# Optimization experiments

Measured on AMD Instinct MI355X. Metric: run time of the kernel, lower is better.

## Reference

```python
import jax, jax.numpy as jnp
import numpy as np

B, D, CL, QL = 32, 128, 1024, 512


def setup_inputs() -> dict:
    key = jax.random.key(0)
    kC, kQ, kW = jax.random.split(key, 3)
    C = jax.random.normal(kC, (B, D, CL), dtype=jnp.float32)
    Q = jax.random.normal(kQ, (B, D, QL), dtype=jnp.float32)
    # xavier_normal_ on (B*CL, 1, 3D): std = sqrt(2 / (fan_in + fan_out)) = sqrt(2/(1+3D))
    std = (2.0 / (1.0 + 3.0 * D)) ** 0.5
    W = jax.random.normal(kW, (B * CL, 1, 3 * D), dtype=jnp.float32) * std
    return {"C": C, "Q": Q, "W": W}


def reference(C, Q, W):
    # C: (B, D, CL), Q: (B, D, QL), W: (B*CL, 1, 3D)
    b, d, cl = C.shape
    Ct = jnp.transpose(C, (0, 2, 1))   # (B, CL, D)
    Qt = jnp.transpose(Q, (0, 2, 1))   # (B, QL, D)
    Wr = W.reshape(b, cl, 3 * d)
    wq, wc, wqc = Wr[..., :d], Wr[..., d:2 * d], Wr[..., 2 * d:]
    # Trilinear similarity: S[b,c,q] = wq[b,c].Q[b,q] + wc[b,c].C[b,c] + wqc[b,c].(C[b,c]*Q[b,q])
    S = (jnp.einsum('bcd,bqd->bcq', wq, Qt)
         + jnp.sum(wc * Ct, axis=-1, keepdims=True)
         + jnp.einsum('bcd,bqd->bcq', wqc * Ct, Qt))   # (B, CL, QL)
    S1 = jax.nn.softmax(S, axis=2)  # over queries
    S2 = jax.nn.softmax(S, axis=1)  # over context
    A = jnp.einsum('bcq,bqd->bcd', S1, Qt)             # (B, CL, D)
    # B = (S1 @ S2^T) @ C, reassociated as S1 @ (S2^T @ C) to avoid (CL,CL) intermediate
    S2tC = jnp.einsum('bkq,bkd->bqd', S2, Ct)          # (B, QL, D)
    Bm = jnp.einsum('bcq,bqd->bcd', S1, S2tC)          # (B, CL, D)
    out = jnp.concatenate([Ct, A, Ct * A, Ct * Bm], axis=2)  # (B, CL, 4D)
    # dropout is identity in eval mode
    return jnp.transpose(out, (0, 2, 1))               # (B, 4D, CL)
```

## Files before the change

kernel.cpp:

```cpp
#include <hip/hip_runtime.h>
#include <hip/hip_bf16.h>
#include <cstddef>

#define B_  32
#define D_  128
#define CL_ 1024
#define QL_ 512

using short8  = __attribute__((ext_vector_type(8))) short;
using short4v = __attribute__((ext_vector_type(4))) short;
using float4v = __attribute__((ext_vector_type(4))) float;

__device__ __forceinline__ unsigned short f2bf(float f) {
    unsigned int u = __float_as_uint(f);
    u += 0x7FFFu + ((u >> 16) & 1u);
    return (unsigned short)(u >> 16);
}
__device__ __forceinline__ float bf2f(unsigned short h) {
    return __uint_as_float(((unsigned int)h) << 16);
}

__global__ __launch_bounds__(256) void k_u_bias(const float* __restrict__ C,
                                                const float* __restrict__ W,
                                                unsigned short* __restrict__ U,
                                                float* __restrict__ bias,
                                                unsigned short* __restrict__ Cbf) {
    int b  = blockIdx.y;
    int c0 = blockIdx.x * 32;
    int tid = threadIdx.x;

    __shared__ float tile[128][33];
    __shared__ float bred[32][9];

    for (int pass = 0; pass < 16; ++pass) {
        int d = pass * 8 + (tid >> 5);
        int c = tid & 31;
        float v = C[((size_t)(b * D_ + d)) * CL_ + c0 + c];
        tile[d][c] = v;
        Cbf[((size_t)(b * D_ + d)) * CL_ + c0 + c] = f2bf(v);
    }
    __syncthreads();

    int tc    = tid >> 3;
    int lane8 = tid & 7;
    int c     = c0 + tc;
    size_t wbase = ((size_t)(b * CL_ + c)) * (3 * D_);
    size_t ubase = ((size_t)(b * CL_ + c)) * D_;

    float bpart = 0.f;
    #pragma unroll
    for (int i = 0; i < 4; ++i) {
        int d = i * 32 + lane8 * 4;
        float4 wq4  = *(const float4*)(W + wbase + d);
        float4 wc4  = *(const float4*)(W + wbase + D_ + d);
        float4 wqc4 = *(const float4*)(W + wbase + 2 * D_ + d);
        float ct0 = tile[d + 0][tc], ct1 = tile[d + 1][tc];
        float ct2 = tile[d + 2][tc], ct3 = tile[d + 3][tc];
        short4v u;
        u[0] = (short)f2bf(wq4.x + wqc4.x * ct0);
        u[1] = (short)f2bf(wq4.y + wqc4.y * ct1);
        u[2] = (short)f2bf(wq4.z + wqc4.z * ct2);
        u[3] = (short)f2bf(wq4.w + wqc4.w * ct3);
        *(short4v*)(U + ubase + d) = u;
        bpart += wc4.x * ct0 + wc4.y * ct1 + wc4.z * ct2 + wc4.w * ct3;
    }
    bred[tc][lane8] = bpart;
    __syncthreads();
    if (lane8 == 0) {
        float s = 0.f;
        for (int i = 0; i < 8; ++i) s += bred[tc][i];
        bias[b * CL_ + c] = s;
    }
}

__global__ __launch_bounds__(256) void k_qt(const float* __restrict__ Q,
                                            unsigned short* __restrict__ Qt,
                                            unsigned short* __restrict__ Qbf) {
    int b  = blockIdx.z;
    int d0 = blockIdx.y * 64;
    int q0 = blockIdx.x * 64;
    int tid = threadIdx.x;
    __shared__ float t[64][65];
    for (int p = 0; p < 16; ++p) {
        int d = p * 4 + (tid >> 6);
        int q = tid & 63;
        float v = Q[((size_t)(b * D_ + d0 + d)) * QL_ + q0 + q];
        t[d][q] = v;
        Qbf[((size_t)(b * D_ + d0 + d)) * QL_ + q0 + q] = f2bf(v);
    }
    __syncthreads();
    for (int p = 0; p < 16; ++p) {
        int q  = p * 4 + (tid >> 6);
        int dd = tid & 63;
        Qt[((size_t)(b * QL_ + q0 + q)) * D_ + d0 + dd] = f2bf(t[dd][q]);
    }
}

__global__ __launch_bounds__(256) void k_gs(const unsigned short* __restrict__ Ubf,
                                            const unsigned short* __restrict__ Qtbf,
                                            const float* __restrict__ bias,
                                            unsigned short* __restrict__ Sbf) {
    int b  = blockIdx.z;
    int m0 = blockIdx.y * 64;
    int n0 = blockIdx.x * 64;

    int tid  = threadIdx.x;
    int lane = tid & 63, wave = tid >> 6;
    int wm = wave >> 1, wn = wave & 1;
    int quad = lane >> 4, l15 = lane & 15;

    __shared__ __align__(16) short As[64][72];
    __shared__ __align__(16) short Bs[64][72];

    const unsigned short* Ab = Ubf  + ((size_t)(b * CL_ + m0)) * D_;
    const unsigned short* Bb = Qtbf + ((size_t)(b * QL_ + n0)) * D_;

    float4v acc[2][2] = {};

    for (int k0 = 0; k0 < D_; k0 += 64) {
        #pragma unroll
        for (int i = 0; i < 2; ++i) {
            int flat = tid + i * 256;
            int row = flat >> 3, col = (flat & 7) * 8;
            *(short8*)&As[row][col] = *(const short8*)(Ab + (size_t)row * D_ + k0 + col);
            *(short8*)&Bs[row][col] = *(const short8*)(Bb + (size_t)row * D_ + k0 + col);
        }
        __syncthreads();
        #pragma unroll
        for (int ks = 0; ks < 64; ks += 32) {
            short8 af0 = *(const short8*)&As[wm * 32 + l15][ks + quad * 8];
            short8 af1 = *(const short8*)&As[wm * 32 + 16 + l15][ks + quad * 8];
            short8 bf0 = *(const short8*)&Bs[wn * 32 + l15][ks + quad * 8];
            short8 bf1 = *(const short8*)&Bs[wn * 32 + 16 + l15][ks + quad * 8];
            acc[0][0] = __builtin_amdgcn_mfma_f32_16x16x32_bf16(af0, bf0, acc[0][0], 0, 0, 0);
            acc[0][1] = __builtin_amdgcn_mfma_f32_16x16x32_bf16(af0, bf1, acc[0][1], 0, 0, 0);
            acc[1][0] = __builtin_amdgcn_mfma_f32_16x16x32_bf16(af1, bf0, acc[1][0], 0, 0, 0);
            acc[1][1] = __builtin_amdgcn_mfma_f32_16x16x32_bf16(af1, bf1, acc[1][1], 0, 0, 0);
        }
        __syncthreads();
    }

    #pragma unroll
    for (int fi = 0; fi < 2; ++fi)
        #pragma unroll
        for (int fj = 0; fj < 2; ++fj)
            #pragma unroll
            for (int rr = 0; rr < 4; ++rr) {
                int m = m0 + wm * 32 + fi * 16 + quad * 4 + rr;
                int nn = n0 + wn * 32 + fj * 16 + l15;
                float v = acc[fi][fj][rr] + bias[b * CL_ + m];
                Sbf[((size_t)(b * CL_ + m)) * QL_ + nn] = f2bf(v);
            }
}

__global__ __launch_bounds__(256) void k_stats(const unsigned short* __restrict__ S,
                                               float* __restrict__ rmax,
                                               float* __restrict__ rinv,
                                               float* __restrict__ pcmax,
                                               float* __restrict__ pcsum) {
    int b     = blockIdx.y;
    int chunk = blockIdx.x;
    int c0    = chunk * 64;
    int tid   = threadIdx.x;

    const unsigned short* Sb = S + (size_t)b * CL_ * QL_;

    float m0 = -1e30f, s0 = 0.f, m1 = -1e30f, s1 = 0.f;
    #pragma unroll 4
    for (int c = 0; c < 64; ++c) {
        unsigned int raw = *(const unsigned int*)(Sb + (size_t)(c0 + c) * QL_ + 2 * tid);
        float v0 = bf2f((unsigned short)(raw & 0xFFFF));
        float v1 = bf2f((unsigned short)(raw >> 16));
        float nm0 = fmaxf(m0, v0);
        s0 = s0 * __expf(m0 - nm0) + __expf(v0 - nm0);
        m0 = nm0;
        float nm1 = fmaxf(m1, v1);
        s1 = s1 * __expf(m1 - nm1) + __expf(v1 - nm1);
        m1 = nm1;
    }
    size_t pbase = ((size_t)(b * 16 + chunk)) * QL_ + 2 * tid;
    *(float2*)(pcmax + pbase) = make_float2(m0, m1);
    *(float2*)(pcsum + pbase) = make_float2(s0, s1);

    int lane = tid & 63, wave = tid >> 6;
    for (int i = 0; i < 16; ++i) {
        int c = c0 + wave * 16 + i;
        const unsigned short* Sr = Sb + (size_t)c * QL_ + lane * 8;
        uint4 raw = *(const uint4*)Sr;
        float v[8];
        v[0] = bf2f(raw.x & 0xFFFF); v[1] = bf2f(raw.x >> 16);
        v[2] = bf2f(raw.y & 0xFFFF); v[3] = bf2f(raw.y >> 16);
        v[4] = bf2f(raw.z & 0xFFFF); v[5] = bf2f(raw.z >> 16);
        v[6] = bf2f(raw.w & 0xFFFF); v[7] = bf2f(raw.w >> 16);
        float m = v[0];
        #pragma unroll
        for (int j = 1; j < 8; ++j) m = fmaxf(m, v[j]);
        for (int off = 32; off; off >>= 1) m = fmaxf(m, __shfl_xor(m, off));
        float s = 0.f;
        #pragma unroll
        for (int j = 0; j < 8; ++j) s += __expf(v[j] - m);
        for (int off = 32; off; off >>= 1) s += __shfl_xor(s, off);
        if (lane == 0) { rmax[b * CL_ + c] = m; rinv[b * CL_ + c] = 1.0f / s; }
    }
}

__global__ __launch_bounds__(256) void k_col_reduce(const float* __restrict__ pcmax,
                                                    const float* __restrict__ pcsum,
                                                    float* __restrict__ cmax,
                                                    float* __restrict__ cinv) {
    int g = blockIdx.x * 256 + threadIdx.x;
    int b = g >> 9, q = g & (QL_ - 1);
    float M = -1e30f, SS = 0.f;
    #pragma unroll
    for (int ch = 0; ch < 16; ++ch) {
        size_t idx = ((size_t)(b * 16 + ch)) * QL_ + q;
        float m = pcmax[idx], s = pcsum[idx];
        float nM = fmaxf(M, m);
        SS = SS * __expf(M - nM) + s * __expf(m - nM);
        M = nM;
    }
    cmax[g] = M;
    cinv[g] = 1.0f / SS;
}

__global__ __launch_bounds__(256) void k_gp(const unsigned short* __restrict__ Cbf,
                                            const unsigned short* __restrict__ Sbf,
                                            const float* __restrict__ cmax,
                                            const float* __restrict__ cinv,
                                            unsigned short* __restrict__ Pbf) {
    int b  = blockIdx.y;
    int q0 = blockIdx.x * 32;

    int tid  = threadIdx.x;
    int lane = tid & 63, wave = tid >> 6;
    int quad = lane >> 4, l15 = lane & 15;

    __shared__ __align__(16) short As[128][72];
    __shared__ __align__(16) short Bs[32][72];
    __shared__ float scm[32], sci[32];

    if (tid < 32) {
        scm[tid] = cmax[b * QL_ + q0 + tid];
        sci[tid] = cinv[b * QL_ + q0 + tid];
    }
    __syncthreads();

    const unsigned short* Cb = Cbf + (size_t)b * D_ * CL_;
    const unsigned short* Sb = Sbf + (size_t)b * CL_ * QL_;

    int arow = tid >> 3;
    int acol = (tid & 7) * 8;
    int srow = tid >> 4;
    int uq   = tid & 15;

    float4v acc[2][2] = {};

    for (int k0 = 0; k0 < CL_; k0 += 64) {
        #pragma unroll
        for (int p = 0; p < 4; ++p) {
            int row = p * 32 + arow;
            *(short8*)&As[row][acol] = *(const short8*)(Cb + (size_t)row * CL_ + k0 + acol);
        }
        #pragma unroll
        for (int p = 0; p < 4; ++p) {
            int crow = p * 16 + srow;
            unsigned int raw = *(const unsigned int*)(Sb + (size_t)(k0 + crow) * QL_ + q0 + 2 * uq);
            float v0 = __expf(bf2f((unsigned short)(raw & 0xFFFF)) - scm[2 * uq]) * sci[2 * uq];
            float v1 = __expf(bf2f((unsigned short)(raw >> 16)) - scm[2 * uq + 1]) * sci[2 * uq + 1];
            Bs[2 * uq][crow]     = (short)f2bf(v0);
            Bs[2 * uq + 1][crow] = (short)f2bf(v1);
        }
        __syncthreads();
        #pragma unroll
        for (int ks = 0; ks < 64; ks += 32) {
            short8 a0 = *(const short8*)&As[wave * 32 + l15][ks + quad * 8];
            short8 a1 = *(const short8*)&As[wave * 32 + 16 + l15][ks + quad * 8];
            short8 b0 = *(const short8*)&Bs[l15][ks + quad * 8];
            short8 b1 = *(const short8*)&Bs[16 + l15][ks + quad * 8];
            acc[0][0] = __builtin_amdgcn_mfma_f32_16x16x32_bf16(a0, b0, acc[0][0], 0, 0, 0);
            acc[0][1] = __builtin_amdgcn_mfma_f32_16x16x32_bf16(a0, b1, acc[0][1], 0, 0, 0);
            acc[1][0] = __builtin_amdgcn_mfma_f32_16x16x32_bf16(a1, b0, acc[1][0], 0, 0, 0);
            acc[1][1] = __builtin_amdgcn_mfma_f32_16x16x32_bf16(a1, b1, acc[1][1], 0, 0, 0);
        }
        __syncthreads();
    }

    #pragma unroll
    for (int fi = 0; fi < 2; ++fi)
        #pragma unroll
        for (int fj = 0; fj < 2; ++fj)
            #pragma unroll
            for (int rr = 0; rr < 4; ++rr) {
                int d = wave * 32 + fi * 16 + quad * 4 + rr;
                int q = q0 + fj * 16 + l15;
                Pbf[((size_t)(b * D_ + d)) * QL_ + q] = f2bf(acc[fi][fj][rr]);
            }
}

template <int PLANE>
__global__ __launch_bounds__(256) void k_av(const unsigned short* __restrict__ A,
                                            const unsigned short* __restrict__ Sbf,
                                            const float* __restrict__ rmax,
                                            const float* __restrict__ rinv,
                                            const float* __restrict__ C,
                                            float* __restrict__ out) {
    int b  = blockIdx.y;
    int n0 = blockIdx.x * 32;

    int tid  = threadIdx.x;
    int lane = tid & 63, wave = tid >> 6;
    int quad = lane >> 4, l15 = lane & 15;

    __shared__ __align__(16) short As[128][72];
    __shared__ __align__(16) short Bs[32][72];
    __shared__ float srm[32], sri[32];

    if (tid < 32) {
        srm[tid] = rmax[b * CL_ + n0 + tid];
        sri[tid] = rinv[b * CL_ + n0 + tid];
    }
    __syncthreads();

    const unsigned short* Ab = A + (size_t)b * D_ * QL_;
    const unsigned short* Sb = Sbf + ((size_t)(b * CL_ + n0)) * QL_;

    int arow = tid >> 3;
    int acol = (tid & 7) * 8;

    float4v acc[2][2] = {};

    for (int k0 = 0; k0 < QL_; k0 += 64) {
        #pragma unroll
        for (int p = 0; p < 4; ++p) {
            int row = p * 32 + arow;
            *(short8*)&As[row][acol] = *(const short8*)(Ab + (size_t)row * QL_ + k0 + acol);
        }
        {
            int brow = tid >> 3;
            uint4 raw = *(const uint4*)(Sb + (size_t)brow * QL_ + k0 + acol);
            unsigned int rw[4] = {raw.x, raw.y, raw.z, raw.w};
            float rm = srm[brow], ri = sri[brow];
            short8 v;
            #pragma unroll
            for (int j = 0; j < 8; ++j) {
                unsigned short bits = (unsigned short)((rw[j >> 1] >> ((j & 1) * 16)) & 0xFFFF);
                v[j] = (short)f2bf(__expf(bf2f(bits) - rm) * ri);
            }
            *(short8*)&Bs[brow][acol] = v;
        }
        __syncthreads();
        #pragma unroll
        for (int ks = 0; ks < 64; ks += 32) {
            short8 a0 = *(const short8*)&As[wave * 32 + l15][ks + quad * 8];
            short8 a1 = *(const short8*)&As[wave * 32 + 16 + l15][ks + quad * 8];
            short8 b0 = *(const short8*)&Bs[l15][ks + quad * 8];
            short8 b1 = *(const short8*)&Bs[16 + l15][ks + quad * 8];
            acc[0][0] = __builtin_amdgcn_mfma_f32_16x16x32_bf16(a0, b0, acc[0][0], 0, 0, 0);
            acc[0][1] = __builtin_amdgcn_mfma_f32_16x16x32_bf16(a0, b1, acc[0][1], 0, 0, 0);
            acc[1][0] = __builtin_amdgcn_mfma_f32_16x16x32_bf16(a1, b0, acc[1][0], 0, 0, 0);
            acc[1][1] = __builtin_amdgcn_mfma_f32_16x16x32_bf16(a1, b1, acc[1][1], 0, 0, 0);
        }
        __syncthreads();
    }

    #pragma unroll
    for (int fi = 0; fi < 2; ++fi)
        #pragma unroll
        for (int fj = 0; fj < 2; ++fj)
            #pragma unroll
            for (int rr = 0; rr < 4; ++rr) {
                int d = wave * 32 + fi * 16 + quad * 4 + rr;
                int c = n0 + fj * 16 + l15;
                float ct = C[((size_t)(b * D_ + d)) * CL_ + c];
                float v  = acc[fi][fj][rr];
                size_t ob = ((size_t)(b * 4 * D_ + d)) * CL_ + c;
                if (PLANE == 0) {
                    out[ob]                        = ct;
                    out[ob + (size_t)D_ * CL_]     = v;
                    out[ob + 2 * (size_t)D_ * CL_] = ct * v;
                } else {
                    out[ob + 3 * (size_t)D_ * CL_] = ct * v;
                }
            }
}

extern "C" void kernel_launch(void* const* d_in, const int* in_sizes, int n_in,
                              void* d_out, int out_size, void* d_ws, size_t ws_size,
                              hipStream_t stream) {
    const float* C = (const float*)d_in[0];
    const float* Q = (const float*)d_in[1];
    const float* W = (const float*)d_in[2];
    float* out = (float*)d_out;

    unsigned short* Ubf  = (unsigned short*)d_ws;
    unsigned short* Qtbf = Ubf  + (size_t)B_ * CL_ * D_;
    unsigned short* Qbf  = Qtbf + (size_t)B_ * QL_ * D_;
    unsigned short* Cbf  = Qbf  + (size_t)B_ * D_ * QL_;
    unsigned short* Pbf  = Cbf  + (size_t)B_ * D_ * CL_;
    unsigned short* Sbf  = Pbf  + (size_t)B_ * D_ * QL_;
    float* bias  = (float*)(Sbf + (size_t)B_ * CL_ * QL_);
    float* rmax  = bias  + (size_t)B_ * CL_;
    float* rinv  = rmax  + (size_t)B_ * CL_;
    float* cmax  = rinv  + (size_t)B_ * CL_;
    float* cinv  = cmax  + (size_t)B_ * QL_;
    float* pcmax = cinv  + (size_t)B_ * QL_;
    float* pcsum = pcmax + (size_t)B_ * 16 * QL_;

    k_u_bias<<<dim3(CL_ / 32, B_), 256, 0, stream>>>(C, W, Ubf, bias, Cbf);
    k_qt<<<dim3(QL_ / 64, D_ / 64, B_), 256, 0, stream>>>(Q, Qtbf, Qbf);
    k_gs<<<dim3(QL_ / 64, CL_ / 64, B_), 256, 0, stream>>>(Ubf, Qtbf, bias, Sbf);
    k_stats<<<dim3(16, B_), 256, 0, stream>>>(Sbf, rmax, rinv, pcmax, pcsum);
    k_col_reduce<<<B_ * QL_ / 256, 256, 0, stream>>>(pcmax, pcsum, cmax, cinv);
    k_gp<<<dim3(QL_ / 32, B_), 256, 0, stream>>>(Cbf, Sbf, cmax, cinv, Pbf);
    k_av<0><<<dim3(CL_ / 32, B_), 256, 0, stream>>>(Qbf, Sbf, rmax, rinv, C, out);
    k_av<1><<<dim3(CL_ / 32, B_), 256, 0, stream>>>(Pbf, Sbf, rmax, rinv, C, out);
}
```

Measured before the change: 228.8 us.

## Fuse similarity GEMM with row and column softmax statistics

Merges the S GEMM kernel and the stats kernel: each block owns a 64-row tile of S for one batch and loops over all 8 query chunks. Row softmax max/sum are kept online in registers, and per-chunk column partial max/sum are written out. This removes the re-read of the bf16 S matrix and one kernel launch. In exchange the grid shrinks from 4096 blocks to 512 and each block runs serially over the query chunks, which lowers parallelism and occupancy.

```diff
diff --git a/kernel.cpp b/kernel.cpp
--- a/kernel.cpp
+++ b/kernel.cpp
@@ -96,38 +96,58 @@
     }
 }
 
-__global__ __launch_bounds__(256) void k_gs(const unsigned short* __restrict__ Ubf,
-                                            const unsigned short* __restrict__ Qtbf,
-                                            const float* __restrict__ bias,
-                                            unsigned short* __restrict__ Sbf) {
-    int b  = blockIdx.z;
-    int m0 = blockIdx.y * 64;
-    int n0 = blockIdx.x * 64;
-
+__global__ __launch_bounds__(256) void k_gs2(const unsigned short* __restrict__ Ubf,
+                                             const unsigned short* __restrict__ Qtbf,
+                                             const float* __restrict__ bias,
+                                             unsigned short* __restrict__ Sbf,
+                                             float* __restrict__ rmax,
+                                             float* __restrict__ rinv,
+                                             float* __restrict__ pcmax,
+                                             float* __restrict__ pcsum) {
+    int mt = blockIdx.x;
+    int b  = blockIdx.y;
+    int m0 = mt * 64;
     int tid  = threadIdx.x;
     int lane = tid & 63, wave = tid >> 6;
     int wm = wave >> 1, wn = wave & 1;
     int quad = lane >> 4, l15 = lane & 15;
 
-    __shared__ __align__(16) short As[64][72];
-    __shared__ __align__(16) short Bs[64][72];
+    __shared__ __align__(16) short As[64][136];
+    __shared__ __align__(16) short Bs[64][136];
+    __shared__ float sbias[64];
+    __shared__ float rmw[2][64], rsw[2][64];
+    __shared__ float cmw[2][64], csw[2][64];
 
     const unsigned short* Ab = Ubf  + ((size_t)(b * CL_ + m0)) * D_;
-    const unsigned short* Bb = Qtbf + ((size_t)(b * QL_ + n0)) * D_;
-
-    float4v acc[2][2] = {};
-
-    for (int k0 = 0; k0 < D_; k0 += 64) {
-        #pragma unroll
-        for (int i = 0; i < 2; ++i) {
+    const unsigned short* Bb = Qtbf + ((size_t)(b * QL_)) * D_;
+
+    #pragma unroll
+    for (int i = 0; i < 4; ++i) {
+        int flat = tid + i * 256;
+        int row = flat >> 4, col = (flat & 15) * 8;
+        *(short8*)&As[row][col] = *(const short8*)(Ab + (size_t)row * D_ + col);
+    }
+    if (tid < 64) sbias[tid] = bias[b * CL_ + m0 + tid];
+
+    float rm_run[2][4], rs_run[2][4];
+    #pragma unroll
+    for (int fi = 0; fi < 2; ++fi)
+        #pragma unroll
+        for (int rr = 0; rr < 4; ++rr) { rm_run[fi][rr] = -1e30f; rs_run[fi][rr] = 0.f; }
+
+    for (int chunk = 0; chunk < 8; ++chunk) {
+        __syncthreads();
+        #pragma unroll
+        for (int i = 0; i < 4; ++i) {
             int flat = tid + i * 256;
-            int row = flat >> 3, col = (flat & 7) * 8;
-            *(short8*)&As[row][col] = *(const short8*)(Ab + (size_t)row * D_ + k0 + col);
-            *(short8*)&Bs[row][col] = *(const short8*)(Bb + (size_t)row * D_ + k0 + col);
-        }
-        __syncthreads();
-        #pragma unroll
-        for (int ks = 0; ks < 64; ks += 32) {
+            int row = flat >> 4, col = (flat & 15) * 8;
+            *(short8*)&Bs[row][col] = *(const short8*)(Bb + (size_t)(chunk * 64 + row) * D_ + col);
+        }
+        __syncthreads();
+
+        float4v acc[2][2] = {};
+        #pragma unroll
+        for (int ks = 0; ks < 128; ks += 32) {
             short8 af0 = *(const short8*)&As[wm * 32 + l15][ks + quad * 8];
             short8 af1 = *(const short8*)&As[wm * 32 + 16 + l15][ks + quad * 8];
             short8 bf0 = *(const short8*)&Bs[wn * 32 + l15][ks + quad * 8];
@@ -137,70 +157,101 @@
             acc[1][0] = __builtin_amdgcn_mfma_f32_16x16x32_bf16(af1, bf0, acc[1][0], 0, 0, 0);
             acc[1][1] = __builtin_amdgcn_mfma_f32_16x16x32_bf16(af1, bf1, acc[1][1], 0, 0, 0);
         }
-        __syncthreads();
-    }
-
-    #pragma unroll
-    for (int fi = 0; fi < 2; ++fi)
-        #pragma unroll
-        for (int fj = 0; fj < 2; ++fj)
+
+        float v[2][2][4];
+        #pragma unroll
+        for (int fi = 0; fi < 2; ++fi)
+            #pragma unroll
+            for (int fj = 0; fj < 2; ++fj)
+                #pragma unroll
+                for (int rr = 0; rr < 4; ++rr) {
+                    int mloc = wm * 32 + fi * 16 + quad * 4 + rr;
+                    float x = acc[fi][fj][rr] + sbias[mloc];
+                    v[fi][fj][rr] = x;
+                    int nloc = wn * 32 + fj * 16 + l15;
+                    Sbf[((size_t)(b * CL_ + m0 + mloc)) * QL_ + chunk * 64 + nloc] = f2bf(x);
+                }
+
+        #pragma unroll
+        for (int fi = 0; fi < 2; ++fi)
             #pragma unroll
             for (int rr = 0; rr < 4; ++rr) {
-                int m = m0 + wm * 32 + fi * 16 + quad * 4 + rr;
-                int nn = n0 + wn * 32 + fj * 16 + l15;
-                float v = acc[fi][fj][rr] + bias[b * CL_ + m];
-                Sbf[((size_t)(b * CL_ + m)) * QL_ + nn] = f2bf(v);
-            }
-}
-
-__global__ __launch_bounds__(256) void k_stats(const unsigned short* __restrict__ S,
-                                               float* __restrict__ rmax,
-                                               float* __restrict__ rinv,
-                                               float* __restrict__ pcmax,
-                                               float* __restrict__ pcsum) {
-    int b     = blockIdx.y;
-    int chunk = blockIdx.x;
-    int c0    = chunk * 64;
-    int tid   = threadIdx.x;
-
-    const unsigned short* Sb = S + (size_t)b * CL_ * QL_;
-
-    float m0 = -1e30f, s0 = 0.f, m1 = -1e30f, s1 = 0.f;
-    #pragma unroll 4
-    for (int c = 0; c < 64; ++c) {
-        unsigned int raw = *(const unsigned int*)(Sb + (size_t)(c0 + c) * QL_ + 2 * tid);
-        float v0 = bf2f((unsigned short)(raw & 0xFFFF));
-        float v1 = bf2f((unsigned short)(raw >> 16));
-        float nm0 = fmaxf(m0, v0);
-        s0 = s0 * __expf(m0 - nm0) + __expf(v0 - nm0);
-        m0 = nm0;
-        float nm1 = fmaxf(m1, v1);
-        s1 = s1 * __expf(m1 - nm1) + __expf(v1 - nm1);
-        m1 = nm1;
-    }
-    size_t pbase = ((size_t)(b * 16 + chunk)) * QL_ + 2 * tid;
-    *(float2*)(pcmax + pbase) = make_float2(m0, m1);
-    *(float2*)(pcsum + pbase) = make_float2(s0, s1);
-
-    int lane = tid & 63, wave = tid >> 6;
-    for (int i = 0; i < 16; ++i) {
-        int c = c0 + wave * 16 + i;
-        const unsigned short* Sr = Sb + (size_t)c * QL_ + lane * 8;
-        uint4 raw = *(const uint4*)Sr;
-        float v[8];
-        v[0] = bf2f(raw.x & 0xFFFF); v[1] = bf2f(raw.x >> 16);
-        v[2] = bf2f(raw.y & 0xFFFF); v[3] = bf2f(raw.y >> 16);
-        v[4] = bf2f(raw.z & 0xFFFF); v[5] = bf2f(raw.z >> 16);
-        v[6] = bf2f(raw.w & 0xFFFF); v[7] = bf2f(raw.w >> 16);
-        float m = v[0];
-        #pragma unroll
-        for (int j = 1; j < 8; ++j) m = fmaxf(m, v[j]);
-        for (int off = 32; off; off >>= 1) m = fmaxf(m, __shfl_xor(m, off));
-        float s = 0.f;
-        #pragma unroll
-        for (int j = 0; j < 8; ++j) s += __expf(v[j] - m);
-        for (int off = 32; off; off >>= 1) s += __shfl_xor(s, off);
-        if (lane == 0) { rmax[b * CL_ + c] = m; rinv[b * CL_ + c] = 1.0f / s; }
+                float v0 = v[fi][0][rr], v1 = v[fi][1][rr];
+                float nm = fmaxf(rm_run[fi][rr], fmaxf(v0, v1));
+                rs_run[fi][rr] = rs_run[fi][rr] * __expf(rm_run[fi][rr] - nm)
+                               + __expf(v0 - nm) + __expf(v1 - nm);
+                rm_run[fi][rr] = nm;
+            }
+
+        #pragma unroll
+        for (int fj = 0; fj < 2; ++fj) {
+            float cm = v[0][fj][0];
+            #pragma unroll
+            for (int fi = 0; fi < 2; ++fi)
+                #pragma unroll
+                for (int rr = 0; rr < 4; ++rr) cm = fmaxf(cm, v[fi][fj][rr]);
+            float cs = 0.f;
+            #pragma unroll
+            for (int fi = 0; fi < 2; ++fi)
+                #pragma unroll
+                for (int rr = 0; rr < 4; ++rr) cs += __expf(v[fi][fj][rr] - cm);
+            #pragma unroll
+            for (int off = 16; off <= 32; off <<= 1) {
+                float om = __shfl_xor(cm, off);
+                float os = __shfl_xor(cs, off);
+                float nm = fmaxf(cm, om);
+                cs = cs * __expf(cm - nm) + os * __expf(om - nm);
+                cm = nm;
+            }
+            if (quad == 0) {
+                int col = wn * 32 + fj * 16 + l15;
+                cmw[wm][col] = cm;
+                csw[wm][col] = cs;
+            }
+        }
+        __syncthreads();
+        if (tid < 64) {
+            float m0v = cmw[0][tid], s0v = csw[0][tid];
+            float m1v = cmw[1][tid], s1v = csw[1][tid];
+            float nm = fmaxf(m0v, m1v);
+            float ss = s0v * __expf(m0v - nm) + s1v * __expf(m1v - nm);
+            size_t pi = ((size_t)(b * 16 + mt)) * QL_ + chunk * 64 + tid;
+            pcmax[pi] = nm;
+            pcsum[pi] = ss;
+        }
+    }
+
+    #pragma unroll
+    for (int off = 1; off <= 8; off <<= 1)
+        #pragma unroll
+        for (int fi = 0; fi < 2; ++fi)
+            #pragma unroll
+            for (int rr = 0; rr < 4; ++rr) {
+                float om = __shfl_xor(rm_run[fi][rr], off);
+                float os = __shfl_xor(rs_run[fi][rr], off);
+                float nm = fmaxf(rm_run[fi][rr], om);
+                rs_run[fi][rr] = rs_run[fi][rr] * __expf(rm_run[fi][rr] - nm)
+                               + os * __expf(om - nm);
+                rm_run[fi][rr] = nm;
+            }
+    if (l15 == 0) {
+        #pragma unroll
+        for (int fi = 0; fi < 2; ++fi)
+            #pragma unroll
+            for (int rr = 0; rr < 4; ++rr) {
+                int m = wm * 32 + fi * 16 + quad * 4 + rr;
+                rmw[wn][m] = rm_run[fi][rr];
+                rsw[wn][m] = rs_run[fi][rr];
+            }
+    }
+    __syncthreads();
+    if (tid < 64) {
+        float m0v = rmw[0][tid], s0v = rsw[0][tid];
+        float m1v = rmw[1][tid], s1v = rsw[1][tid];
+        float nm = fmaxf(m0v, m1v);
+        float ss = s0v * __expf(m0v - nm) + s1v * __expf(m1v - nm);
+        rmax[b * CL_ + m0 + tid] = nm;
+        rinv[b * CL_ + m0 + tid] = 1.0f / ss;
     }
 }
 
@@ -408,8 +459,7 @@
 
     k_u_bias<<<dim3(CL_ / 32, B_), 256, 0, stream>>>(C, W, Ubf, bias, Cbf);
     k_qt<<<dim3(QL_ / 64, D_ / 64, B_), 256, 0, stream>>>(Q, Qtbf, Qbf);
-    k_gs<<<dim3(QL_ / 64, CL_ / 64, B_), 256, 0, stream>>>(Ubf, Qtbf, bias, Sbf);
-    k_stats<<<dim3(16, B_), 256, 0, stream>>>(Sbf, rmax, rinv, pcmax, pcsum);
+    k_gs2<<<dim3(16, B_), 256, 0, stream>>>(Ubf, Qtbf, bias, Sbf, rmax, rinv, pcmax, pcsum);
     k_col_reduce<<<B_ * QL_ / 256, 256, 0, stream>>>(pcmax, pcsum, cmax, cinv);
     k_gp<<<dim3(QL_ / 32, B_), 256, 0, stream>>>(Cbf, Sbf, cmax, cinv, Pbf);
     k_av<0><<<dim3(CL_ / 32, B_), 256, 0, stream>>>(Qbf, Sbf, rmax, rinv, C, out);
```

New measurement: 205.4 us. -10.2%, faster.
